# Optimization experiments

Hardware: AMD Instinct MI355X
Metric: run time of the kernel (lower is better)

Reference implementation:

```python
import jax, jax.numpy as jnp
import numpy as np

K = 512      # per-token feature dim (also per-head dim in this module)
H = 8        # heads
B = 2
T = 2048


def setup_inputs() -> dict:
    key = jax.random.key(0)
    ks = jax.random.split(key, 6)
    s = 1.0 / np.sqrt(K)
    x = jax.random.normal(ks[0], (B, T, K), dtype=jnp.float32)
    # torch Linear(k, k*heads, bias=False): y = x @ W with W stored here as [in, out]
    Wq = jax.random.uniform(ks[1], (K, K * H), dtype=jnp.float32, minval=-s, maxval=s)
    Wk = jax.random.uniform(ks[2], (K, K * H), dtype=jnp.float32, minval=-s, maxval=s)
    Wv = jax.random.uniform(ks[3], (K, K * H), dtype=jnp.float32, minval=-s, maxval=s)
    su = 1.0 / np.sqrt(K * H)
    Wu = jax.random.uniform(ks[4], (K * H, K), dtype=jnp.float32, minval=-su, maxval=su)
    bu = jax.random.uniform(ks[5], (K,), dtype=jnp.float32, minval=-su, maxval=su)
    return {"x": x, "Wq": Wq, "Wk": Wk, "Wv": Wv, "Wu": Wu, "bu": bu}


def reference(x, Wq, Wk, Wv, Wu, bu):
    b, t, k = x.shape
    h = H
    # project and split heads: [b, t, h, k] -> [b, h, t, k]
    q = (x @ Wq).reshape(b, t, h, k).transpose(0, 2, 1, 3)
    kk = (x @ Wk).reshape(b, t, h, k).transpose(0, 2, 1, 3)
    v = (x @ Wv).reshape(b, t, h, k).transpose(0, 2, 1, 3)
    scale = k ** (-0.25)  # applied to both q and k, matching source
    dot = jnp.einsum('bhqd,bhkd->bhqk', q * scale, kk * scale)
    attn = jax.nn.softmax(dot, axis=-1)
    out = jnp.einsum('bhqk,bhkd->bhqd', attn, v)          # [b, h, t, k]
    out = out.transpose(0, 2, 1, 3).reshape(b, t, h * k)   # [b, t, h*k]
    return out @ Wu + bu
```

## Files before the change

### kernel.cpp

```cpp
#include <hip/hip_runtime.h>

typedef unsigned short u16;
typedef unsigned short ushort8 __attribute__((ext_vector_type(8)));
typedef unsigned short us4 __attribute__((ext_vector_type(4)));
typedef __bf16 bf16x8 __attribute__((ext_vector_type(8)));
typedef float f32x4 __attribute__((ext_vector_type(4)));

#define DEV static __device__ __forceinline__

DEV u16 f2bf(float f) {
    unsigned int u = __builtin_bit_cast(unsigned int, f);
    u += 0x7FFFu + ((u >> 16) & 1u);
    return (u16)(u >> 16);
}

DEV f32x4 mfma16(ushort8 a, ushort8 b, f32x4 c) {
    return __builtin_amdgcn_mfma_f32_16x16x32_bf16((bf16x8)a, (bf16x8)b, c, 0, 0, 0);
}

DEV void gload_lds16(const void* g, void* l) {
    __builtin_amdgcn_global_load_lds(
        (const __attribute__((address_space(1))) void*)g,
        (__attribute__((address_space(3))) void*)l, 16, 0, 0);
}

__global__ void cvt_kernel(const float* __restrict__ in, u16* __restrict__ out, int n) {
    int i = (blockIdx.x * 256 + threadIdx.x) * 4;
    if (i >= n) return;
    float4 f = *(const float4*)(in + i);
    us4 o;
    o.x = f2bf(f.x); o.y = f2bf(f.y); o.z = f2bf(f.z); o.w = f2bf(f.w);
    *(us4*)(out + i) = o;
}

__global__ void transpose_cvt(const float* __restrict__ in, u16* __restrict__ out, int R, int C) {
    __shared__ u16 tile[64][72];
    int c0 = blockIdx.x << 6, r0 = blockIdx.y << 6;
    int tx = threadIdx.x & 63, ty = threadIdx.x >> 6;
    for (int i = 0; i < 64; i += 4) {
        int r = i + ty;
        tile[r][tx] = f2bf(in[(size_t)(r0 + r) * C + c0 + tx]);
    }
    __syncthreads();
    for (int i = 0; i < 64; i += 4) {
        int r = i + ty;
        out[(size_t)(c0 + r) * R + r0 + tx] = tile[tx][r];
    }
}

__global__ void transpose_cvt3(const float* __restrict__ in0, const float* __restrict__ in1,
                               const float* __restrict__ in2, u16* __restrict__ outbase) {
    __shared__ u16 tile[64][72];
    const float* in = (blockIdx.z == 0) ? in0 : (blockIdx.z == 1) ? in1 : in2;
    u16* out = outbase + (size_t)blockIdx.z * 2097152;
    const int R = 512, C = 4096;
    int c0 = blockIdx.x << 6, r0 = blockIdx.y << 6;
    int tx = threadIdx.x & 63, ty = threadIdx.x >> 6;
    for (int i = 0; i < 64; i += 4) {
        int r = i + ty;
        tile[r][tx] = f2bf(in[(size_t)(r0 + r) * C + c0 + tx]);
    }
    __syncthreads();
    for (int i = 0; i < 64; i += 4) {
        int r = i + ty;
        out[(size_t)(c0 + r) * R + r0 + tx] = tile[tx][r];
    }
}

__global__ void transpose_bh(const u16* __restrict__ in, u16* __restrict__ out) {
    __shared__ u16 tile[64][72];
    int bh = blockIdx.z;
    int d0 = blockIdx.x << 6, t0 = blockIdx.y << 6;
    int tx = threadIdx.x & 63, ty = threadIdx.x >> 6;
    const u16* src = in + (size_t)bh * 2048 * 512;
    u16* dst = out + (size_t)bh * 512 * 2048;
    for (int i = 0; i < 64; i += 4) {
        int r = i + ty;
        tile[r][tx] = src[(size_t)(t0 + r) * 512 + d0 + tx];
    }
    __syncthreads();
    for (int i = 0; i < 64; i += 4) {
        int r = i + ty;
        dst[(size_t)(d0 + r) * 2048 + t0 + tx] = tile[tx][r];
    }
}

__launch_bounds__(256, 3)
__global__ void gemm_qkv(const u16* __restrict__ A, const u16* __restrict__ Btbase,
                         float s2, u16* __restrict__ outbase) {
    __shared__ u16 Asub[128 * 32];
    __shared__ u16 Bsub[128 * 32];
    const int Kc = 512;
    const u16* Bt = Btbase + (size_t)blockIdx.z * 2097152;
    u16* out = outbase + (size_t)blockIdx.z * 16777216;
    const float scale = (blockIdx.z == 0) ? s2 : 1.0f;

    const int tid = threadIdx.x, lane = tid & 63, wv = tid >> 6;
    const int bm = blockIdx.y << 7, bn = blockIdx.x << 7;
    const int wr = (wv >> 1) << 6, wc = (wv & 1) << 6;
    const int lr = lane & 15, hi = lane >> 4;

    f32x4 acc[4][4] = {};

    int off0 = (wv * 2048 + lane * 16) >> 1;
    int row0 = off0 >> 5, k0e = off0 & 31;
    int off1 = off0 + 512;
    int row1 = off1 >> 5, k1e = off1 & 31;

    const u16* Ag0 = A + (size_t)(bm + row0) * Kc + k0e;
    const u16* Ag1 = A + (size_t)(bm + row1) * Kc + k1e;
    const u16* Bg0 = Bt + (size_t)(bn + row0) * Kc + k0e;
    const u16* Bg1 = Bt + (size_t)(bn + row1) * Kc + k1e;

    for (int kk = 0; kk < Kc; kk += 32) {
        __syncthreads();
        gload_lds16(Ag0 + kk, &Asub[wv * 1024]);
        gload_lds16(Ag1 + kk, &Asub[wv * 1024 + 512]);
        gload_lds16(Bg0 + kk, &Bsub[wv * 1024]);
        gload_lds16(Bg1 + kk, &Bsub[wv * 1024 + 512]);
        __syncthreads();

        ushort8 a[4], b[4];
#pragma unroll
        for (int m = 0; m < 4; ++m)
            a[m] = *(const ushort8*)&Asub[(wr + m * 16 + lr) * 32 + hi * 8];
#pragma unroll
        for (int n = 0; n < 4; ++n)
            b[n] = *(const ushort8*)&Bsub[(wc + n * 16 + lr) * 32 + hi * 8];
#pragma unroll
        for (int m = 0; m < 4; ++m)
#pragma unroll
            for (int n = 0; n < 4; ++n)
                acc[m][n] = mfma16(a[m], b[n], acc[m][n]);
    }

#pragma unroll
    for (int m = 0; m < 4; ++m)
#pragma unroll
        for (int n = 0; n < 4; ++n)
#pragma unroll
            for (int r = 0; r < 4; ++r) {
                int row = bm + wr + m * 16 + hi * 4 + r;
                int col = bn + wc + n * 16 + lr;
                float v = acc[m][n][r] * scale;
                size_t dst = ((size_t)((row >> 11) * 8 + (col >> 9)) * 2048 + (row & 2047)) * 512
                             + (col & 511);
                out[dst] = f2bf(v);
            }
}

__launch_bounds__(256, 3)
__global__ void gemm_final(const u16* __restrict__ A, const u16* __restrict__ Bt,
                           const float* __restrict__ bias, float* __restrict__ out, int Kc) {
    __shared__ u16 Asub[128 * 32];
    __shared__ u16 Bsub[64 * 32];
    const int tid = threadIdx.x, lane = tid & 63, wv = tid >> 6;
    const int bm = blockIdx.y << 7, bn = blockIdx.x << 6;
    const int wr = (wv >> 1) << 6, wc = (wv & 1) << 5;
    const int lr = lane & 15, hi = lane >> 4;

    f32x4 acc[4][2] = {};

    const u16* gsrc[3];
    u16* ldst[3];
#pragma unroll
    for (int j = 0; j < 3; ++j) {
        int g = wv * 3 + j;
        int off = g * 512 + lane * 8;
        if (g < 8) {
            int row = off >> 5, k = off & 31;
            gsrc[j] = A + (size_t)(bm + row) * Kc + k;
            ldst[j] = &Asub[g * 512];
        } else {
            int off2 = off - 4096;
            int row = off2 >> 5, k = off2 & 31;
            gsrc[j] = Bt + (size_t)(bn + row) * Kc + k;
            ldst[j] = &Bsub[(g - 8) * 512];
        }
    }

    for (int kk = 0; kk < Kc; kk += 32) {
        __syncthreads();
#pragma unroll
        for (int j = 0; j < 3; ++j) gload_lds16(gsrc[j] + kk, ldst[j]);
        __syncthreads();

        ushort8 a[4], b[2];
#pragma unroll
        for (int m = 0; m < 4; ++m)
            a[m] = *(const ushort8*)&Asub[(wr + m * 16 + lr) * 32 + hi * 8];
#pragma unroll
        for (int n = 0; n < 2; ++n)
            b[n] = *(const ushort8*)&Bsub[(wc + n * 16 + lr) * 32 + hi * 8];
#pragma unroll
        for (int m = 0; m < 4; ++m)
#pragma unroll
            for (int n = 0; n < 2; ++n)
                acc[m][n] = mfma16(a[m], b[n], acc[m][n]);
    }

#pragma unroll
    for (int m = 0; m < 4; ++m)
#pragma unroll
        for (int n = 0; n < 2; ++n)
#pragma unroll
            for (int r = 0; r < 4; ++r) {
                int row = bm + wr + m * 16 + hi * 4 + r;
                int col = bn + wc + n * 16 + lr;
                out[(size_t)row * 512 + col] = acc[m][n][r] + bias[col];
            }
}

__launch_bounds__(512, 2)
__global__ void attn_kernel(const u16* __restrict__ Q, const u16* __restrict__ K,
                            const u16* __restrict__ Vt, u16* __restrict__ O) {
    __shared__ u16 Klds[2][32 * 512];
    __shared__ u16 Plds[2][128 * 40];
    __shared__ __align__(16) float red[2][128];
    __shared__ __align__(16) float lred[128];
    __shared__ int rflag[2][8];

    const int tid = threadIdx.x, lane = tid & 63, wv = tid >> 6;
    const int lr = lane & 15, hi = lane >> 4;
    const int qh = wv >> 2, ds = wv & 3;

    const int flat = blockIdx.x;
    const int nid = (flat & 7) * 32 + (flat >> 3);
    const int bh = nid >> 4;
    const int q0 = (nid & 15) << 7;

    ushort8 qf[16];
    {
        const char* Qg = (const char*)(Q + ((size_t)bh * 2048 + q0 + wv * 16 + lr) * 512) + hi * 16;
#pragma unroll
        for (int ks = 0; ks < 16; ++ks) qf[ks] = *(const ushort8*)(Qg + ks * 64);
    }

    f32x4 acc[4][8] = {};
    float mrun = -1e30f, lrun = 0.f;

    const char* Kg = (const char*)(K + (size_t)bh * 2048 * 512);
    const char* Vg = (const char*)(Vt + (size_t)bh * 512 * 2048);

    auto s_phase = [&](const char* Kb, f32x4& s0, f32x4& s1) {
        s0 = (f32x4){0.f, 0.f, 0.f, 0.f};
        s1 = (f32x4){0.f, 0.f, 0.f, 0.f};
#pragma unroll
        for (int ks = 0; ks < 16; ++ks) {
            int swz = (ks * 64 + hi * 16) ^ ((lr & 7) << 4);
            ushort8 kf0 = *(const ushort8*)(Kb + lr * 1024 + swz);
            ushort8 kf1 = *(const ushort8*)(Kb + (lr + 16) * 1024 + swz);
            s0 = mfma16(kf0, qf[ks], s0);
            s1 = mfma16(kf1, qf[ks], s1);
        }
    };

    auto softmax_store = [&](const f32x4& s0, const f32x4& s1, int pcb) {
        float mx = fmaxf(fmaxf(fmaxf(s0[0], s0[1]), fmaxf(s0[2], s0[3])),
                         fmaxf(fmaxf(s1[0], s1[1]), fmaxf(s1[2], s1[3])));
        mx = fmaxf(mx, __shfl_xor(mx, 16));
        mx = fmaxf(mx, __shfl_xor(mx, 32));
        float a = 1.0f;
        bool upd = false;
        if (mx > mrun + 11.5f) { a = exp2f(mrun - mx); mrun = mx; upd = true; }
        float p[8];
#pragma unroll
        for (int r = 0; r < 4; ++r) {
            p[r]     = exp2f(s0[r] - mrun);
            p[4 + r] = exp2f(s1[r] - mrun);
        }
        float ps = ((p[0] + p[1]) + (p[2] + p[3])) + ((p[4] + p[5]) + (p[6] + p[7]));
        ps += __shfl_xor(ps, 16);
        ps += __shfl_xor(ps, 32);
        lrun = lrun * a + ps;

        const int qr = wv * 16 + lr;
        char* Pb = (char*)&Plds[pcb][0] + qr * 80;
        uint2 w01, w23;
        w01.x = (unsigned)f2bf(p[0]) | ((unsigned)f2bf(p[1]) << 16);
        w01.y = (unsigned)f2bf(p[2]) | ((unsigned)f2bf(p[3]) << 16);
        w23.x = (unsigned)f2bf(p[4]) | ((unsigned)f2bf(p[5]) << 16);
        w23.y = (unsigned)f2bf(p[6]) | ((unsigned)f2bf(p[7]) << 16);
        *(uint2*)(Pb + hi * 8) = w01;
        *(uint2*)(Pb + 32 + hi * 8) = w23;
        if (hi == 0) red[pcb][qr] = a;
        if (lane == 0) rflag[pcb][wv] = __any(upd) ? 1 : 0;
    };

    auto pv_phase = [&](int pcb, int ktv) {
        int anyupd = rflag[pcb][0] | rflag[pcb][1] | rflag[pcb][2] | rflag[pcb][3]
                   | rflag[pcb][4] | rflag[pcb][5] | rflag[pcb][6] | rflag[pcb][7];
        if (anyupd) {
#pragma unroll
            for (int mf = 0; mf < 4; ++mf) {
                f32x4 a4 = *(const f32x4*)&red[pcb][qh * 64 + mf * 16 + hi * 4];
#pragma unroll
                for (int nf = 0; nf < 8; ++nf)
#pragma unroll
                    for (int r = 0; r < 4; ++r) acc[mf][nf][r] *= a4[r];
            }
        }
        ushort8 pf[4];
#pragma unroll
        for (int mf = 0; mf < 4; ++mf)
            pf[mf] = *(const ushort8*)((const char*)&Plds[pcb][0]
                                       + (qh * 64 + mf * 16 + lr) * 80 + hi * 16);
        __builtin_amdgcn_s_setprio(1);
#pragma unroll
        for (int nf = 0; nf < 8; ++nf) {
            int d = ds * 128 + nf * 16 + lr;
            ushort8 vf = *(const ushort8*)(Vg + (size_t)d * 4096 + (size_t)ktv * 2 + hi * 16);
#pragma unroll
            for (int mf = 0; mf < 4; ++mf) acc[mf][nf] = mfma16(pf[mf], vf, acc[mf][nf]);
        }
        __builtin_amdgcn_s_setprio(0);
    };

    auto prefetch_k = [&](int tt) {
        const char* Kgt = Kg + (size_t)tt * 32 * 1024;
#pragma unroll
        for (int r4 = 0; r4 < 4; ++r4) {
            int r = wv * 4 + r4;
            gload_lds16(Kgt + (size_t)r * 1024 + ((lane ^ (r & 7)) << 4),
                        &Klds[tt & 1][(size_t)r * 512]);
        }
    };

    f32x4 s0c, s1c, s0p, s1p;

    prefetch_k(0);
    __syncthreads();

    prefetch_k(1);
    s_phase((const char*)&Klds[0][0], s0c, s1c);
    __syncthreads();

    for (int t = 1; t < 64; ++t) {
        if (t + 1 < 64) prefetch_k(t + 1);

        s0p = s0c; s1p = s1c;
        s_phase((const char*)&Klds[t & 1][0], s0c, s1c);
        softmax_store(s0p, s1p, (t - 1) & 1);

        __syncthreads();

        pv_phase((t - 1) & 1, (t - 1) << 5);
    }

    softmax_store(s0c, s1c, 1);
    __syncthreads();
    pv_phase(1, 63 << 5);

    if (hi == 0) lred[wv * 16 + lr] = lrun;
    __syncthreads();

    const int b = bh >> 3, h = bh & 7;
#pragma unroll
    for (int mf = 0; mf < 4; ++mf) {
        f32x4 lv = *(const f32x4*)&lred[qh * 64 + mf * 16 + hi * 4];
        f32x4 inv;
#pragma unroll
        for (int r = 0; r < 4; ++r) inv[r] = 1.0f / lv[r];
#pragma unroll
        for (int nf = 0; nf < 8; ++nf) {
            int d = ds * 128 + nf * 16 + lr;
#pragma unroll
            for (int r = 0; r < 4; ++r) {
                int t = q0 + qh * 64 + mf * 16 + hi * 4 + r;
                O[((size_t)(b * 2048 + t)) * 4096 + h * 512 + d] = f2bf(acc[mf][nf][r] * inv[r]);
            }
        }
    }
}

extern "C" void kernel_launch(void* const* d_in, const int* in_sizes, int n_in,
                              void* d_out, int out_size, void* d_ws, size_t ws_size,
                              hipStream_t stream) {
    const float* x  = (const float*)d_in[0];
    const float* Wq = (const float*)d_in[1];
    const float* Wk = (const float*)d_in[2];
    const float* Wv = (const float*)d_in[3];
    const float* Wu = (const float*)d_in[4];
    const float* bu = (const float*)d_in[5];

    char* ws = (char*)d_ws;
    const size_t MB = 1ull << 20;
    u16* xb  = (u16*)(ws + 0);
    u16* Wqt = (u16*)(ws + 4 * MB);
    u16* Wut = (u16*)(ws + 16 * MB);
    u16* Qb  = (u16*)(ws + 20 * MB);
    u16* Kb  = (u16*)(ws + 52 * MB);
    u16* Vb  = (u16*)(ws + 84 * MB);
    u16* Vtb = (u16*)(ws + 116 * MB);
    u16* Ob  = (u16*)(ws + 84 * MB);

    cvt_kernel<<<2048, 256, 0, stream>>>(x, xb, 2 * 2048 * 512);
    transpose_cvt3<<<dim3(64, 8, 3), 256, 0, stream>>>(Wq, Wk, Wv, Wqt);
    transpose_cvt<<<dim3(8, 64), 256, 0, stream>>>(Wu, Wut, 4096, 512);

    const float s2 = 0.06375871593f;
    gemm_qkv<<<dim3(32, 32, 3), 256, 0, stream>>>(xb, Wqt, s2, Qb);

    transpose_bh<<<dim3(8, 32, 16), 256, 0, stream>>>(Vb, Vtb);

    attn_kernel<<<256, 512, 0, stream>>>(Qb, Kb, Vtb, Ob);

    gemm_final<<<dim3(8, 32), 256, 0, stream>>>(Ob, Wut, bu, (float*)d_out, 4096);
}
```

Before: 469.1 us.

## Merge prep conversions into one kernel and write V transposed from QKV GEMM

Combines the x conversion and the three weight transpose-convert launches into a single prep kernel dispatched by block index. The QKV GEMM epilogue for the V slice now writes directly into the transposed [b,h,d,t] layout with packed 4-element stores, which removes the separate transpose_bh pass and its 32MB round trip. This saves launch overhead and memory traffic. The cost is a transposed epilogue whose stores stride across t and may coalesce less well than the original row-major writes.

Result: faster. 457.0 us (median of 2 runs) (-2.6%).

```diff
diff --git a/kernel.cpp b/kernel.cpp
--- a/kernel.cpp
+++ b/kernel.cpp
@@ -24,18 +24,38 @@
         (__attribute__((address_space(3))) void*)l, 16, 0, 0);
 }
 
-__global__ void cvt_kernel(const float* __restrict__ in, u16* __restrict__ out, int n) {
-    int i = (blockIdx.x * 256 + threadIdx.x) * 4;
-    if (i >= n) return;
-    float4 f = *(const float4*)(in + i);
-    us4 o;
-    o.x = f2bf(f.x); o.y = f2bf(f.y); o.z = f2bf(f.z); o.w = f2bf(f.w);
-    *(us4*)(out + i) = o;
-}
-
-__global__ void transpose_cvt(const float* __restrict__ in, u16* __restrict__ out, int R, int C) {
+__global__ void prep_kernel(const float* __restrict__ x,
+                            const float* __restrict__ Wq, const float* __restrict__ Wk,
+                            const float* __restrict__ Wv, const float* __restrict__ Wu,
+                            u16* __restrict__ xb, u16* __restrict__ Wqt, u16* __restrict__ Wut) {
     __shared__ u16 tile[64][72];
-    int c0 = blockIdx.x << 6, r0 = blockIdx.y << 6;
+    const int bid = blockIdx.x;
+
+    if (bid < 2048) {
+        int i = (bid * 256 + threadIdx.x) * 4;
+        float4 f = *(const float4*)(x + i);
+        us4 o;
+        o.x = f2bf(f.x); o.y = f2bf(f.y); o.z = f2bf(f.z); o.w = f2bf(f.w);
+        *(us4*)(xb + i) = o;
+        return;
+    }
+
+    const float* in;
+    u16* out;
+    int R, C, c0, r0;
+    if (bid < 3584) {
+        int j = bid - 2048;
+        int z = j >> 9, rem = j & 511;
+        in = (z == 0) ? Wq : (z == 1) ? Wk : Wv;
+        out = Wqt + (size_t)z * 2097152;
+        R = 512; C = 4096;
+        c0 = (rem & 63) << 6; r0 = (rem >> 6) << 6;
+    } else {
+        int k = bid - 3584;
+        in = Wu; out = Wut;
+        R = 4096; C = 512;
+        c0 = (k & 7) << 6; r0 = (k >> 3) << 6;
+    }
     int tx = threadIdx.x & 63, ty = threadIdx.x >> 6;
     for (int i = 0; i < 64; i += 4) {
         int r = i + ty;
@@ -48,46 +68,9 @@
     }
 }
 
-__global__ void transpose_cvt3(const float* __restrict__ in0, const float* __restrict__ in1,
-                               const float* __restrict__ in2, u16* __restrict__ outbase) {
-    __shared__ u16 tile[64][72];
-    const float* in = (blockIdx.z == 0) ? in0 : (blockIdx.z == 1) ? in1 : in2;
-    u16* out = outbase + (size_t)blockIdx.z * 2097152;
-    const int R = 512, C = 4096;
-    int c0 = blockIdx.x << 6, r0 = blockIdx.y << 6;
-    int tx = threadIdx.x & 63, ty = threadIdx.x >> 6;
-    for (int i = 0; i < 64; i += 4) {
-        int r = i + ty;
-        tile[r][tx] = f2bf(in[(size_t)(r0 + r) * C + c0 + tx]);
-    }
-    __syncthreads();
-    for (int i = 0; i < 64; i += 4) {
-        int r = i + ty;
-        out[(size_t)(c0 + r) * R + r0 + tx] = tile[tx][r];
-    }
-}
-
-__global__ void transpose_bh(const u16* __restrict__ in, u16* __restrict__ out) {
-    __shared__ u16 tile[64][72];
-    int bh = blockIdx.z;
-    int d0 = blockIdx.x << 6, t0 = blockIdx.y << 6;
-    int tx = threadIdx.x & 63, ty = threadIdx.x >> 6;
-    const u16* src = in + (size_t)bh * 2048 * 512;
-    u16* dst = out + (size_t)bh * 512 * 2048;
-    for (int i = 0; i < 64; i += 4) {
-        int r = i + ty;
-        tile[r][tx] = src[(size_t)(t0 + r) * 512 + d0 + tx];
-    }
-    __syncthreads();
-    for (int i = 0; i < 64; i += 4) {
-        int r = i + ty;
-        dst[(size_t)(d0 + r) * 2048 + t0 + tx] = tile[tx][r];
-    }
-}
-
 __launch_bounds__(256, 3)
 __global__ void gemm_qkv(const u16* __restrict__ A, const u16* __restrict__ Btbase,
-                         float s2, u16* __restrict__ outbase) {
+                         float s2, u16* __restrict__ outbase, u16* __restrict__ vtb) {
     __shared__ u16 Asub[128 * 32];
     __shared__ u16 Bsub[128 * 32];
     const int Kc = 512;
@@ -134,19 +117,35 @@
                 acc[m][n] = mfma16(a[m], b[n], acc[m][n]);
     }
 
-#pragma unroll
-    for (int m = 0; m < 4; ++m)
-#pragma unroll
-        for (int n = 0; n < 4; ++n)
-#pragma unroll
-            for (int r = 0; r < 4; ++r) {
-                int row = bm + wr + m * 16 + hi * 4 + r;
-                int col = bn + wc + n * 16 + lr;
-                float v = acc[m][n][r] * scale;
-                size_t dst = ((size_t)((row >> 11) * 8 + (col >> 9)) * 2048 + (row & 2047)) * 512
-                             + (col & 511);
-                out[dst] = f2bf(v);
+    if (blockIdx.z == 2) {
+#pragma unroll
+        for (int m = 0; m < 4; ++m)
+#pragma unroll
+            for (int n = 0; n < 4; ++n) {
+                int row0v = bm + wr + m * 16 + hi * 4;
+                int col   = bn + wc + n * 16 + lr;
+                int b = row0v >> 11, t0 = row0v & 2047;
+                int h = col >> 9, d = col & 511;
+                us4 pk;
+#pragma unroll
+                for (int r = 0; r < 4; ++r) pk[r] = f2bf(acc[m][n][r]);
+                *(us4*)&vtb[(((size_t)(b * 8 + h) * 512 + d) << 11) + t0] = pk;
             }
+    } else {
+#pragma unroll
+        for (int m = 0; m < 4; ++m)
+#pragma unroll
+            for (int n = 0; n < 4; ++n)
+#pragma unroll
+                for (int r = 0; r < 4; ++r) {
+                    int row = bm + wr + m * 16 + hi * 4 + r;
+                    int col = bn + wc + n * 16 + lr;
+                    float v = acc[m][n][r] * scale;
+                    size_t dst = ((size_t)((row >> 11) * 8 + (col >> 9)) * 2048 + (row & 2047)) * 512
+                                 + (col & 511);
+                    out[dst] = f2bf(v);
+                }
+    }
 }
 
 __launch_bounds__(256, 3)
@@ -390,18 +389,13 @@
     u16* Wut = (u16*)(ws + 16 * MB);
     u16* Qb  = (u16*)(ws + 20 * MB);
     u16* Kb  = (u16*)(ws + 52 * MB);
-    u16* Vb  = (u16*)(ws + 84 * MB);
     u16* Vtb = (u16*)(ws + 116 * MB);
     u16* Ob  = (u16*)(ws + 84 * MB);
 
-    cvt_kernel<<<2048, 256, 0, stream>>>(x, xb, 2 * 2048 * 512);
-    transpose_cvt3<<<dim3(64, 8, 3), 256, 0, stream>>>(Wq, Wk, Wv, Wqt);
-    transpose_cvt<<<dim3(8, 64), 256, 0, stream>>>(Wu, Wut, 4096, 512);
+    prep_kernel<<<4096, 256, 0, stream>>>(x, Wq, Wk, Wv, Wu, xb, Wqt, Wut);
 
     const float s2 = 0.06375871593f;
-    gemm_qkv<<<dim3(32, 32, 3), 256, 0, stream>>>(xb, Wqt, s2, Qb);
-
-    transpose_bh<<<dim3(8, 32, 16), 256, 0, stream>>>(Vb, Vtb);
+    gemm_qkv<<<dim3(32, 32, 3), 256, 0, stream>>>(xb, Wqt, s2, Qb, Vtb);
 
     attn_kernel<<<256, 512, 0, stream>>>(Qb, Kb, Vtb, Ob);
 
```
